# Kernel optimization log

Measured on AMD Instinct MI355X. Metric: run time of the kernel, lower is better.

The kernel has to match this reference:

```python
import jax, jax.numpy as jnp
import numpy as np

NUM_HEADS = 16


def setup_inputs() -> dict:
    key = jax.random.key(0)
    ks = jax.random.split(key, 5)
    B, S, D = 2, 2048, 1024
    x = jax.random.normal(ks[0], (B, S, D), dtype=jnp.float32)
    # Linear weights stored torch-style as [out, in]; init scale ~ 1/sqrt(D)
    scale = 1.0 / np.sqrt(D)
    Wq = jax.random.uniform(ks[1], (D, D), jnp.float32, -scale, scale)
    bq = jax.random.uniform(ks[2], (D,), jnp.float32, -scale, scale)
    Wo = jax.random.uniform(ks[3], (D, D), jnp.float32, -scale, scale)
    bo = jax.random.uniform(ks[4], (D,), jnp.float32, -scale, scale)
    return {"x": x, "Wq": Wq, "bq": bq, "Wo": Wo, "bo": bo}


def reference(x, Wq, bq, Wo, bo):
    B, S, D = x.shape
    H = NUM_HEADS
    Hd = D // H
    # NOTE: faithful to the source bug — Q, K, V all use the *query* projection.
    q = x @ Wq.T + bq                       # [B,S,D]
    qh = q.reshape(B, S, H, Hd).transpose(0, 2, 1, 3)  # [B,H,S,Hd]
    scores = jnp.einsum('bhsd,bhtd->bhst', qh, qh) / jnp.sqrt(jnp.float32(Hd))
    weights = jax.nn.softmax(scores, axis=-1)          # [B,H,S,S]
    attn = jnp.einsum('bhst,bhtd->bhsd', weights, qh)  # [B,H,S,Hd]
    attn = attn.transpose(0, 2, 1, 3).reshape(B, S, D)
    return attn @ Wo.T + bo
```

## Files before the change

### kernel.cpp

```cpp
#include <hip/hip_runtime.h>
#include <hip/hip_bf16.h>

typedef __bf16 bf16x8 __attribute__((ext_vector_type(8)));
typedef float  f32x4  __attribute__((ext_vector_type(4)));
typedef float  f32x16 __attribute__((ext_vector_type(16)));

__device__ __forceinline__ void gload_lds16(const void* g, void* l) {
  __builtin_amdgcn_global_load_lds(
      (const __attribute__((address_space(1))) unsigned int*)g,
      (__attribute__((address_space(3))) unsigned int*)l, 16, 0, 0);
}

__device__ __forceinline__ void xcd_remap(int& x, int& y) {
  const int lin = blockIdx.x + (blockIdx.y << 4);
  const int xcd = lin & 7, slot = lin >> 3;
  y = ((slot >> 4) << 3) + xcd;
  x = slot & 15;
}

__global__ void k_cvt(const float* __restrict__ s, __bf16* __restrict__ d, int n4) {
  int i = blockIdx.x * blockDim.x + threadIdx.x;
  if (i >= n4) return;
  float4 v = ((const float4*)s)[i];
  union { __bf16 h[4]; uint2 u; } o;
  o.h[0] = (__bf16)v.x; o.h[1] = (__bf16)v.y;
  o.h[2] = (__bf16)v.z; o.h[3] = (__bf16)v.w;
  ((uint2*)d)[i] = o.u;
}

template<bool OUT_BF16>
__global__ __launch_bounds__(256, 2)
void k_gemm_bt(const __bf16* __restrict__ A, const __bf16* __restrict__ B,
               const float* __restrict__ bias, void* __restrict__ C,
               int M, int N, int K) {
  __shared__ __align__(16) __bf16 At[4][128 * 32];
  __shared__ __align__(16) __bf16 Bt[4][64 * 32];
  const int tid  = threadIdx.x;
  const int lane = tid & 63;
  const int w    = tid >> 6;
  const int wr   = w >> 1, wc = w & 1;
  int bx, by; xcd_remap(bx, by);
  const int bm = by * 128, bn = bx * 64;

  f32x4 acc[4][2] = {};

  const __bf16* ga = A + (size_t)(bm + (tid >> 2)) * K + (tid & 3) * 8;
  const __bf16* gb = B + (size_t)(bn + (tid >> 2)) * K + (tid & 3) * 8;

#pragma unroll
  for (int p = 0; p < 2; ++p) {
    gload_lds16(ga + p * 32,                  &At[p][(w * 16) * 32]);
    gload_lds16(ga + p * 32 + (size_t)64 * K, &At[p][(64 + w * 16) * 32]);
    gload_lds16(gb + p * 32,                  &Bt[p][(w * 16) * 32]);
  }

  const int NIT = K / 32;
  for (int it = 0; it < NIT; ++it) {
    const int cur = it & 3;
    if (it + 2 < NIT) {
      const int nb = (it + 2) & 3;
      const int k2 = (it + 2) * 32;
      gload_lds16(ga + k2,                  &At[nb][(w * 16) * 32]);
      gload_lds16(ga + k2 + (size_t)64 * K, &At[nb][(64 + w * 16) * 32]);
      gload_lds16(gb + k2,                  &Bt[nb][(w * 16) * 32]);
      asm volatile("s_waitcnt vmcnt(6)" ::: "memory");
    } else if (it + 2 == NIT) {
      asm volatile("s_waitcnt vmcnt(3)" ::: "memory");
    } else {
      asm volatile("s_waitcnt vmcnt(0)" ::: "memory");
    }
    __builtin_amdgcn_s_barrier();
    __builtin_amdgcn_sched_barrier(0);

    bf16x8 a[4], b[2];
#pragma unroll
    for (int mt = 0; mt < 4; ++mt)
      a[mt] = *(const bf16x8*)&At[cur][(wr * 64 + mt * 16 + (lane & 15)) * 32 + (lane >> 4) * 8];
#pragma unroll
    for (int nt = 0; nt < 2; ++nt)
      b[nt] = *(const bf16x8*)&Bt[cur][(wc * 32 + nt * 16 + (lane & 15)) * 32 + (lane >> 4) * 8];
    __builtin_amdgcn_s_setprio(1);
#pragma unroll
    for (int mt = 0; mt < 4; ++mt)
#pragma unroll
      for (int nt = 0; nt < 2; ++nt)
        acc[mt][nt] = __builtin_amdgcn_mfma_f32_16x16x32_bf16(a[mt], b[nt], acc[mt][nt], 0, 0, 0);
    __builtin_amdgcn_s_setprio(0);
  }

#pragma unroll
  for (int nt = 0; nt < 2; ++nt) {
    const int col = bn + wc * 32 + nt * 16 + (lane & 15);
    const float bv = bias[col];
#pragma unroll
    for (int mt = 0; mt < 4; ++mt) {
#pragma unroll
      for (int r = 0; r < 4; ++r) {
        const int row = bm + wr * 64 + mt * 16 + (lane >> 4) * 4 + r;
        const float v = acc[mt][nt][r] + bv;
        if (OUT_BF16) ((__bf16*)C)[(size_t)row * N + col] = (__bf16)v;
        else          ((float*)C)[(size_t)row * N + col]  = v;
      }
    }
  }
}

#define SWZ2(row, col) ((row) * 64 + ((col) ^ (((((row) & 7) ^ ((row) >> 3)) & 7) << 3)))

#define ATTN_TILE(T, KB, VB)                                                  \
  {                                                                           \
    *(bf16x8*)&KB[SWZ2(2 * sm, c0)]     = v0;                                 \
    *(bf16x8*)&KB[SWZ2(2 * sm + 1, c0)] = v1;                                 \
    _Pragma("unroll")                                                         \
    for (int j = 0; j < 8; ++j) {                                             \
      union { __bf16 b[2]; unsigned u; } pk;                                  \
      pk.b[0] = v0[j]; pk.b[1] = v1[j];                                       \
      *(unsigned*)&VB[SWZ2(c0 + j, 2 * sm)] = pk.u;                           \
    }                                                                         \
    __syncthreads();                                                          \
    if ((T) < 31) {                                                           \
      v0 = *(const bf16x8*)&gsrc[(size_t)((T) + 1) * 64 * 1024];              \
      v1 = *(const bf16x8*)&gsrc[(size_t)((T) + 1) * 64 * 1024 + 1024];       \
    }                                                                         \
    f32x16 s[2] = {};                                                         \
    _Pragma("unroll")                                                         \
    for (int kvf = 0; kvf < 2; ++kvf) {                                       \
      __builtin_amdgcn_s_setprio(1);                                          \
      _Pragma("unroll")                                                       \
      for (int ks = 0; ks < 4; ++ks) {                                        \
        bf16x8 ka = *(const bf16x8*)&KB[SWZ2(kvf * 32 + l31, ks * 16 + h * 8)]; \
        s[kvf] = __builtin_amdgcn_mfma_f32_32x32x16_bf16(ka, qb[ks], s[kvf], 0, 0, 0); \
      }                                                                       \
      __builtin_amdgcn_s_setprio(0);                                          \
    }                                                                         \
    unsigned P[2][4][2];                                                      \
    _Pragma("unroll")                                                         \
    for (int kvf = 0; kvf < 2; ++kvf) {                                       \
      _Pragma("unroll")                                                       \
      for (int rq = 0; rq < 4; ++rq) {                                        \
        _Pragma("unroll")                                                     \
        for (int tt = 0; tt < 2; ++tt) {                                      \
          const float p0 = __builtin_amdgcn_exp2f(s[kvf][rq * 4 + tt * 2]);   \
          const float p1 = __builtin_amdgcn_exp2f(s[kvf][rq * 4 + tt * 2 + 1]); \
          union { __bf16 b[2]; unsigned u; } pk;                              \
          pk.b[0] = (__bf16)p0; pk.b[1] = (__bf16)p1;                         \
          P[kvf][rq][tt] = pk.u;                                              \
        }                                                                     \
      }                                                                       \
    }                                                                         \
    _Pragma("unroll")                                                         \
    for (int ko = 0; ko < 4; ++ko) {                                          \
      const int kvf = ko >> 1, rqa = (ko & 1) * 2, rqb = rqa + 1;             \
      asm volatile("v_permlane32_swap_b32 %0, %1"                             \
                   : "+v"(P[kvf][rqa][0]), "+v"(P[kvf][rqb][0]));             \
      asm volatile("v_permlane32_swap_b32 %0, %1"                             \
                   : "+v"(P[kvf][rqa][1]), "+v"(P[kvf][rqb][1]));             \
    }                                                                         \
    __builtin_amdgcn_s_setprio(1);                                            \
    _Pragma("unroll")                                                         \
    for (int ko = 0; ko < 4; ++ko) {                                          \
      const int kvf = ko >> 1, rqa = (ko & 1) * 2, rqb = rqa + 1;             \
      union { unsigned u[4]; bf16x8 v; } pu;                                  \
      pu.u[0] = P[kvf][rqa][0]; pu.u[1] = P[kvf][rqa][1];                     \
      pu.u[2] = P[kvf][rqb][0]; pu.u[3] = P[kvf][rqb][1];                     \
      Osum = __builtin_amdgcn_mfma_f32_32x32x16_bf16(pu.v, onesb, Osum, 0, 0, 0); \
      bf16x8 vb0 = *(const bf16x8*)&VB[SWZ2(l31,      ko * 16 + h * 8)];      \
      bf16x8 vb1 = *(const bf16x8*)&VB[SWZ2(32 + l31, ko * 16 + h * 8)];      \
      O[0] = __builtin_amdgcn_mfma_f32_32x32x16_bf16(pu.v, vb0, O[0], 0, 0, 0); \
      O[1] = __builtin_amdgcn_mfma_f32_32x32x16_bf16(pu.v, vb1, O[1], 0, 0, 0); \
    }                                                                         \
    __builtin_amdgcn_s_setprio(0);                                            \
  }

__global__ __launch_bounds__(256, 2)
void k_attn(const __bf16* __restrict__ q, __bf16* __restrict__ o) {
  __shared__ __align__(16) __bf16 Kt[2][64 * 64];
  __shared__ __align__(16) __bf16 Vt[2][64 * 64];
  const int tid = threadIdx.x, lane = tid & 63;
  const int w = tid >> 6;
  const int l31 = lane & 31, h = lane >> 5;
  int bqx, bh; xcd_remap(bqx, bh);
  const size_t base = ((size_t)(bh >> 4) * 2048) * 1024 + (bh & 15) * 64;
  const int q0 = bqx * 128 + w * 32;
  const float c2 = 0.18033688f;

  union { unsigned u[4]; bf16x8 v; } ones_u;
  ones_u.u[0] = 0x3F803F80u; ones_u.u[1] = 0x3F803F80u;
  ones_u.u[2] = 0x3F803F80u; ones_u.u[3] = 0x3F803F80u;
  const bf16x8 onesb = ones_u.v;

  bf16x8 qb[4];
#pragma unroll
  for (int ks = 0; ks < 4; ++ks) {
    union { bf16x8 v; __bf16 b[8]; } u;
    u.v = *(const bf16x8*)&q[base + (size_t)(q0 + l31) * 1024 + ks * 16 + h * 8];
#pragma unroll
    for (int j = 0; j < 8; ++j) u.b[j] = (__bf16)((float)u.b[j] * c2);
    qb[ks] = u.v;
  }

  f32x16 O[2] = {};
  f32x16 Osum = {};

  const int sm = tid >> 3, c0 = (tid & 7) * 8;
  const __bf16* gsrc = q + base + (size_t)(2 * sm) * 1024 + c0;

  __bf16* const K0 = &Kt[0][0];  __bf16* const V0 = &Vt[0][0];
  __bf16* const K1 = &Kt[1][0];  __bf16* const V1 = &Vt[1][0];

  bf16x8 v0 = *(const bf16x8*)&gsrc[0];
  bf16x8 v1 = *(const bf16x8*)&gsrc[1024];

  for (int t2 = 0; t2 < 16; ++t2) {
    ATTN_TILE(2 * t2,     K0, V0)
    ATTN_TILE(2 * t2 + 1, K1, V1)
  }

#pragma unroll
  for (int r = 0; r < 16; ++r) {
    const int qrow = (r & 3) + 8 * (r >> 2) + 4 * h;
    const float rs = 1.0f / Osum[r];
    o[base + (size_t)(q0 + qrow) * 1024 + l31]      = (__bf16)(O[0][r] * rs);
    o[base + (size_t)(q0 + qrow) * 1024 + 32 + l31] = (__bf16)(O[1][r] * rs);
  }
}

extern "C" void kernel_launch(void* const* d_in, const int* in_sizes, int n_in,
                              void* d_out, int out_size, void* d_ws, size_t ws_size,
                              hipStream_t stream) {
  const float* x  = (const float*)d_in[0];
  const float* Wq = (const float*)d_in[1];
  const float* bq = (const float*)d_in[2];
  const float* Wo = (const float*)d_in[3];
  const float* bo = (const float*)d_in[4];

  char* ws = (char*)d_ws;
  __bf16* xb  = (__bf16*)(ws);
  __bf16* ab  = (__bf16*)(ws);
  __bf16* wqb = (__bf16*)(ws + ((size_t)8  << 20));
  __bf16* wob = (__bf16*)(ws + ((size_t)10 << 20));
  __bf16* qb  = (__bf16*)(ws + ((size_t)12 << 20));

  const int M = 4096, N = 1024, K = 1024;

  k_cvt<<<(M * K / 4 + 255) / 256, 256, 0, stream>>>(x,  xb,  M * K / 4);
  k_cvt<<<(N * K / 4 + 255) / 256, 256, 0, stream>>>(Wq, wqb, N * K / 4);
  k_cvt<<<(N * K / 4 + 255) / 256, 256, 0, stream>>>(Wo, wob, N * K / 4);

  k_gemm_bt<true ><<<dim3(16, 32), 256, 0, stream>>>(xb, wqb, bq, qb, M, N, K);
  k_attn          <<<dim3(16, 32), 256, 0, stream>>>(qb, ab);
  k_gemm_bt<false><<<dim3(16, 32), 256, 0, stream>>>(ab, wob, bo, d_out, M, N, K);
}
```

Measured before the change: 98.56 us.

## Merge conversion kernels and retile GEMMs to 128x128 with 32x32 MFMA

The three fp32-to-bf16 conversion launches become one combined kernel, saving launch overhead. Both projection GEMMs move from 128x64 to 128x128 block tiles, use 32x32x16 MFMA instructions and an XOR-swizzled LDS layout, and get a new XCD-aware block mapping. The larger tile raises operand reuse and cuts bank conflicts. In exchange the launch grid halves to 256 blocks and occupancy is lowered to one block per CU, which may leave parts of the GPU underfed.

```diff
diff --git a/kernel.cpp b/kernel.cpp
--- a/kernel.cpp
+++ b/kernel.cpp
@@ -18,86 +18,106 @@
   x = slot & 15;
 }
 
-__global__ void k_cvt(const float* __restrict__ s, __bf16* __restrict__ d, int n4) {
-  int i = blockIdx.x * blockDim.x + threadIdx.x;
-  if (i >= n4) return;
-  float4 v = ((const float4*)s)[i];
+__global__ void k_cvt3(const float* __restrict__ x, const float* __restrict__ wq,
+                       const float* __restrict__ wo, __bf16* __restrict__ xb,
+                       __bf16* __restrict__ wqb, __bf16* __restrict__ wob) {
+  const int i = blockIdx.x * 256 + threadIdx.x;
+  const float* s; __bf16* d; int j;
+  if (i < 1048576)      { s = x;  d = xb;  j = i; }
+  else if (i < 1310720) { s = wq; d = wqb; j = i - 1048576; }
+  else                  { s = wo; d = wob; j = i - 1310720; }
+  float4 v = ((const float4*)s)[j];
   union { __bf16 h[4]; uint2 u; } o;
   o.h[0] = (__bf16)v.x; o.h[1] = (__bf16)v.y;
   o.h[2] = (__bf16)v.z; o.h[3] = (__bf16)v.w;
-  ((uint2*)d)[i] = o.u;
+  ((uint2*)d)[j] = o.u;
 }
 
 template<bool OUT_BF16>
-__global__ __launch_bounds__(256, 2)
+__global__ __launch_bounds__(256, 1)
 void k_gemm_bt(const __bf16* __restrict__ A, const __bf16* __restrict__ B,
                const float* __restrict__ bias, void* __restrict__ C,
                int M, int N, int K) {
   __shared__ __align__(16) __bf16 At[4][128 * 32];
-  __shared__ __align__(16) __bf16 Bt[4][64 * 32];
+  __shared__ __align__(16) __bf16 Bt[4][128 * 32];
   const int tid  = threadIdx.x;
   const int lane = tid & 63;
   const int w    = tid >> 6;
   const int wr   = w >> 1, wc = w & 1;
-  int bx, by; xcd_remap(bx, by);
-  const int bm = by * 128, bn = bx * 64;
-
-  f32x4 acc[4][2] = {};
-
-  const __bf16* ga = A + (size_t)(bm + (tid >> 2)) * K + (tid & 3) * 8;
-  const __bf16* gb = B + (size_t)(bn + (tid >> 2)) * K + (tid & 3) * 8;
-
-#pragma unroll
-  for (int p = 0; p < 2; ++p) {
-    gload_lds16(ga + p * 32,                  &At[p][(w * 16) * 32]);
-    gload_lds16(ga + p * 32 + (size_t)64 * K, &At[p][(64 + w * 16) * 32]);
-    gload_lds16(gb + p * 32,                  &Bt[p][(w * 16) * 32]);
-  }
+  const int l31  = lane & 31, h = lane >> 5;
+  const int lin = blockIdx.x + (blockIdx.y << 3);
+  const int xcd = lin & 7, slot = lin >> 3;
+  const int bm = (xcd * 4 + (slot >> 3)) * 128;
+  const int bn = (slot & 7) * 128;
+
+  f32x16 acc[2][2] = {};
+
+  const int kg = (((lane & 3) ^ ((lane >> 2) & 3)) << 3);
+  const __bf16* ga = A + (size_t)(bm + w * 16 + (lane >> 2)) * K + kg;
+  const __bf16* gb = B + (size_t)(bn + w * 16 + (lane >> 2)) * K + kg;
+
+#define STAGE(buf, k0)                                                  \
+  gload_lds16(ga + (k0),                  &At[buf][w * 512]);           \
+  gload_lds16(ga + (k0) + (size_t)64 * K, &At[buf][2048 + w * 512]);    \
+  gload_lds16(gb + (k0),                  &Bt[buf][w * 512]);           \
+  gload_lds16(gb + (k0) + (size_t)64 * K, &Bt[buf][2048 + w * 512]);
+
+  STAGE(0, 0)
+  STAGE(1, 32)
 
   const int NIT = K / 32;
   for (int it = 0; it < NIT; ++it) {
     const int cur = it & 3;
     if (it + 2 < NIT) {
-      const int nb = (it + 2) & 3;
-      const int k2 = (it + 2) * 32;
-      gload_lds16(ga + k2,                  &At[nb][(w * 16) * 32]);
-      gload_lds16(ga + k2 + (size_t)64 * K, &At[nb][(64 + w * 16) * 32]);
-      gload_lds16(gb + k2,                  &Bt[nb][(w * 16) * 32]);
-      asm volatile("s_waitcnt vmcnt(6)" ::: "memory");
+      STAGE((it + 2) & 3, (it + 2) * 32)
+      asm volatile("s_waitcnt vmcnt(8)" ::: "memory");
     } else if (it + 2 == NIT) {
-      asm volatile("s_waitcnt vmcnt(3)" ::: "memory");
+      asm volatile("s_waitcnt vmcnt(4)" ::: "memory");
     } else {
       asm volatile("s_waitcnt vmcnt(0)" ::: "memory");
     }
     __builtin_amdgcn_s_barrier();
     __builtin_amdgcn_sched_barrier(0);
 
-    bf16x8 a[4], b[2];
-#pragma unroll
-    for (int mt = 0; mt < 4; ++mt)
-      a[mt] = *(const bf16x8*)&At[cur][(wr * 64 + mt * 16 + (lane & 15)) * 32 + (lane >> 4) * 8];
-#pragma unroll
-    for (int nt = 0; nt < 2; ++nt)
-      b[nt] = *(const bf16x8*)&Bt[cur][(wc * 32 + nt * 16 + (lane & 15)) * 32 + (lane >> 4) * 8];
+    bf16x8 a[2][2], b[2][2];
+#pragma unroll
+    for (int af = 0; af < 2; ++af)
+#pragma unroll
+      for (int ks = 0; ks < 2; ++ks) {
+        const int row = wr * 64 + af * 32 + l31;
+        const int col = (ks * 16 + h * 8) ^ ((l31 & 3) << 3);
+        a[af][ks] = *(const bf16x8*)&At[cur][row * 32 + col];
+      }
+#pragma unroll
+    for (int bf = 0; bf < 2; ++bf)
+#pragma unroll
+      for (int ks = 0; ks < 2; ++ks) {
+        const int row = wc * 64 + bf * 32 + l31;
+        const int col = (ks * 16 + h * 8) ^ ((l31 & 3) << 3);
+        b[bf][ks] = *(const bf16x8*)&Bt[cur][row * 32 + col];
+      }
     __builtin_amdgcn_s_setprio(1);
 #pragma unroll
-    for (int mt = 0; mt < 4; ++mt)
-#pragma unroll
-      for (int nt = 0; nt < 2; ++nt)
-        acc[mt][nt] = __builtin_amdgcn_mfma_f32_16x16x32_bf16(a[mt], b[nt], acc[mt][nt], 0, 0, 0);
+    for (int ks = 0; ks < 2; ++ks)
+#pragma unroll
+      for (int af = 0; af < 2; ++af)
+#pragma unroll
+        for (int bf = 0; bf < 2; ++bf)
+          acc[af][bf] = __builtin_amdgcn_mfma_f32_32x32x16_bf16(a[af][ks], b[bf][ks], acc[af][bf], 0, 0, 0);
     __builtin_amdgcn_s_setprio(0);
   }
-
-#pragma unroll
-  for (int nt = 0; nt < 2; ++nt) {
-    const int col = bn + wc * 32 + nt * 16 + (lane & 15);
+#undef STAGE
+
+#pragma unroll
+  for (int bf = 0; bf < 2; ++bf) {
+    const int col = bn + wc * 64 + bf * 32 + l31;
     const float bv = bias[col];
 #pragma unroll
-    for (int mt = 0; mt < 4; ++mt) {
-#pragma unroll
-      for (int r = 0; r < 4; ++r) {
-        const int row = bm + wr * 64 + mt * 16 + (lane >> 4) * 4 + r;
-        const float v = acc[mt][nt][r] + bv;
+    for (int af = 0; af < 2; ++af) {
+#pragma unroll
+      for (int r = 0; r < 16; ++r) {
+        const int row = bm + wr * 64 + af * 32 + (r & 3) + 8 * (r >> 2) + 4 * h;
+        const float v = acc[af][bf][r] + bv;
         if (OUT_BF16) ((__bf16*)C)[(size_t)row * N + col] = (__bf16)v;
         else          ((float*)C)[(size_t)row * N + col]  = v;
       }
@@ -243,11 +263,9 @@
 
   const int M = 4096, N = 1024, K = 1024;
 
-  k_cvt<<<(M * K / 4 + 255) / 256, 256, 0, stream>>>(x,  xb,  M * K / 4);
-  k_cvt<<<(N * K / 4 + 255) / 256, 256, 0, stream>>>(Wq, wqb, N * K / 4);
-  k_cvt<<<(N * K / 4 + 255) / 256, 256, 0, stream>>>(Wo, wob, N * K / 4);
-
-  k_gemm_bt<true ><<<dim3(16, 32), 256, 0, stream>>>(xb, wqb, bq, qb, M, N, K);
+  k_cvt3<<<6144, 256, 0, stream>>>(x, Wq, Wo, xb, wqb, wob);
+
+  k_gemm_bt<true ><<<dim3(8, 32), 256, 0, stream>>>(xb, wqb, bq, qb, M, N, K);
   k_attn          <<<dim3(16, 32), 256, 0, stream>>>(qb, ab);
-  k_gemm_bt<false><<<dim3(16, 32), 256, 0, stream>>>(ab, wob, bo, d_out, M, N, K);
-}
+  k_gemm_bt<false><<<dim3(8, 32), 256, 0, stream>>>(ab, wob, bo, d_out, M, N, K);
+}
```

Result: slower. 103.1 us (+4.6%).
